# Kernel optimization log

Measured on AMD Instinct MI355X. Metric: run time of the kernel, lower is better.

Reference implementation:

```python
import jax, jax.numpy as jnp
import numpy as np

DIM = 768      # model dim (c_s)
C_PAIR = 128   # pair channels (c_z)
H = 16         # heads
C = DIM // H   # per-head dim (48)
INF = 1e8
EPS = 1e-5


def _ln(x, w=None, b=None):
    mu = jnp.mean(x, axis=-1, keepdims=True)
    var = jnp.mean(jnp.square(x - mu), axis=-1, keepdims=True)
    y = (x - mu) * jax.lax.rsqrt(var + EPS)
    if w is not None:
        y = y * w
    if b is not None:
        y = y + b
    return y


def setup_inputs() -> dict:
    key = jax.random.key(0)
    ks = jax.random.split(key, 12)
    B, S, N = 1, 2, 1024
    sd = 1.0 / np.sqrt(DIM)
    return {
        "single_repr": jax.random.normal(ks[0], (B, S, N, DIM), jnp.float32),
        "single_proj": jax.random.normal(ks[1], (B, S, N, DIM), jnp.float32),
        "pair_repr": jax.random.normal(ks[2], (B, N, N, C_PAIR), jnp.float32),
        "mask": jnp.ones((B, N), jnp.float32),
        # AdaLN params: LN(a) has no affine; LN(s) is scale-only; gate Linear + skip LinearNoBias
        "adaln_s_w": jnp.ones((DIM,), jnp.float32),
        "adaln_gate_w": (jax.random.normal(ks[3], (DIM, DIM), jnp.float32) * sd),
        "adaln_gate_b": jnp.zeros((DIM,), jnp.float32),
        "adaln_skip_w": (jax.random.normal(ks[4], (DIM, DIM), jnp.float32) * sd),
        # Attention params (q/k/v no bias, sigmoid gate linear, output linear)
        "wq": jax.random.normal(ks[5], (DIM, DIM), jnp.float32) * sd,
        "wk": jax.random.normal(ks[6], (DIM, DIM), jnp.float32) * sd,
        "wv": jax.random.normal(ks[7], (DIM, DIM), jnp.float32) * sd,
        "w_gate": jax.random.normal(ks[8], (DIM, DIM), jnp.float32) * sd,
        "b_gate": jnp.ones((DIM,), jnp.float32),
        "wo": jax.random.normal(ks[9], (DIM, DIM), jnp.float32) * sd,
        "bo": jnp.zeros((DIM,), jnp.float32),
        # proj_pair_bias: LayerNorm(c_pair) + LinearNoBias(c_pair, H)
        "pair_ln_w": jnp.ones((C_PAIR,), jnp.float32),
        "pair_ln_b": jnp.zeros((C_PAIR,), jnp.float32),
        "w_pair": jax.random.normal(ks[10], (C_PAIR, H), jnp.float32) / np.sqrt(C_PAIR),
        # output gating linear (bias initialized to -2 as in the module)
        "w_out": jax.random.normal(ks[11], (DIM, DIM), jnp.float32) * sd,
        "b_out": jnp.full((DIM,), -2.0, jnp.float32),
    }


def reference(single_repr, single_proj, pair_repr, mask,
              adaln_s_w, adaln_gate_w, adaln_gate_b, adaln_skip_w,
              wq, wk, wv, w_gate, b_gate, wo, bo,
              pair_ln_w, pair_ln_b, w_pair, w_out, b_out):
    B, S, N, _ = single_repr.shape
    # AdaLN input gating: a = sigmoid(Lin(LN_scale(s))) * LN(a) + LinNoBias(LN_scale(s))
    a = _ln(single_repr)
    s = _ln(single_proj, adaln_s_w)
    a = jax.nn.sigmoid(s @ adaln_gate_w + adaln_gate_b) * a + s @ adaln_skip_w
    # Biases: mask_bias [B,1,1,1,N]; pair_bias [B,1,H,N,N]
    mask_bias = (INF * (mask - 1.0))[:, None, None, None, :]
    pair_bias = _ln(pair_repr, pair_ln_w, pair_ln_b) @ w_pair      # [B,N,N,H]
    pair_bias = jnp.transpose(pair_bias, (0, 3, 1, 2))[:, None]    # [B,1,H,N,N]
    # Multi-head attention with fused biases
    q = (a @ wq).reshape(B, S, N, H, C)
    k = (a @ wk).reshape(B, S, N, H, C)
    v = (a @ wv).reshape(B, S, N, H, C)
    scale = 1.0 / np.sqrt(C)
    scores = jnp.einsum('bsqhc,bskhc->bshqk', q, k) * scale + mask_bias + pair_bias
    attn = jax.nn.softmax(scores, axis=-1)
    o = jnp.einsum('bshqk,bskhc->bsqhc', attn, v).reshape(B, S, N, DIM)
    # sigmoid gating on attention output, then output projection
    o = o * jax.nn.sigmoid(a @ w_gate + b_gate)
    o = o @ wo + bo
    # final sigmoid output gating (input_gating=True)
    out = jax.nn.sigmoid(o @ w_out + b_out) * o
    return out
```

## Files before the change

### kernel.cpp

```cpp
#include <hip/hip_runtime.h>

#define NROWS 2048
#define NN    1024
#define DIMM  768
#define HEADS 16
#define CH    48
#define CPAIR 128

typedef unsigned short u16;
typedef unsigned int   u32;
typedef __attribute__((ext_vector_type(8))) short short8;
typedef __attribute__((ext_vector_type(4))) float f32x4;

__device__ __forceinline__ float sigm(float x){ return 1.0f/(1.0f+__expf(-x)); }
__device__ __forceinline__ u16 f2bf(float x){
    u32 u = __float_as_uint(x);
    u32 r = u + 0x7FFFu + ((u>>16)&1u);
    return (u16)(r>>16);
}
__device__ __forceinline__ float bf2f(u16 h){ return __uint_as_float(((u32)h)<<16); }
__device__ __forceinline__ void bfsplit(float x, u16& hi, u16& lo){
    hi = f2bf(x);
    lo = f2bf(x - bf2f(hi));
}

__global__ __launch_bounds__(256) void k_ln_single(
    const float* __restrict__ srep, const float* __restrict__ sproj,
    const float* __restrict__ sw, float* __restrict__ a_ln,
    u16* __restrict__ shi, u16* __restrict__ slo)
{
    int r = blockIdx.x, t = threadIdx.x;
    const float* xa = srep  + (size_t)r*DIMM;
    const float* xs = sproj + (size_t)r*DIMM;
    float va[3], vs[3];
    float sa=0.f,qa=0.f,ss=0.f,qs=0.f;
    #pragma unroll
    for (int i=0;i<3;i++){ float x=xa[t+256*i]; va[i]=x; sa+=x; qa+=x*x; }
    #pragma unroll
    for (int i=0;i<3;i++){ float x=xs[t+256*i]; vs[i]=x; ss+=x; qs+=x*x; }
    #pragma unroll
    for (int off=32; off>=1; off>>=1){
        sa += __shfl_xor(sa,off); qa += __shfl_xor(qa,off);
        ss += __shfl_xor(ss,off); qs += __shfl_xor(qs,off);
    }
    __shared__ float red[16];
    int w = t>>6;
    if ((t&63)==0){ red[w*4+0]=sa; red[w*4+1]=qa; red[w*4+2]=ss; red[w*4+3]=qs; }
    __syncthreads();
    sa = red[0]+red[4]+red[8]+red[12];
    qa = red[1]+red[5]+red[9]+red[13];
    ss = red[2]+red[6]+red[10]+red[14];
    qs = red[3]+red[7]+red[11]+red[15];
    float mua=sa*(1.f/768.f), mus=ss*(1.f/768.f);
    float rva=rsqrtf(fmaxf(qa*(1.f/768.f)-mua*mua,0.f)+1e-5f);
    float rvs=rsqrtf(fmaxf(qs*(1.f/768.f)-mus*mus,0.f)+1e-5f);
    #pragma unroll
    for (int i=0;i<3;i++){
        int c=t+256*i;
        size_t idx=(size_t)r*DIMM+c;
        a_ln[idx]=(va[i]-mua)*rva;
        float sv=(vs[i]-mus)*rvs*sw[c];
        u16 h,l; bfsplit(sv,h,l);
        shi[idx]=h; slo[idx]=l;
    }
}

__global__ __launch_bounds__(256) void k_wsplit(
    const float* __restrict__ w0, const float* __restrict__ w1,
    const float* __restrict__ w2, const float* __restrict__ w3,
    const float* __restrict__ w4, const float* __restrict__ w5,
    const float* __restrict__ w6, const float* __restrict__ w7,
    u16* __restrict__ wt)
{
    __shared__ float tile[64][68];
    int n0 = blockIdx.x*64, k0 = blockIdx.y*64, z = blockIdx.z;
    const float* src;
    switch(z){
        case 0: src=w0; break; case 1: src=w1; break;
        case 2: src=w2; break; case 3: src=w3; break;
        case 4: src=w4; break; case 5: src=w5; break;
        case 6: src=w6; break; default: src=w7; break;
    }
    int t = threadIdx.x;
    #pragma unroll
    for (int it=0; it<4; it++){
        int idx = t + it*256;
        int kr = idx>>4, nc = (idx&15)*4;
        float4 v = *(const float4*)(src + (size_t)(k0+kr)*DIMM + n0+nc);
        *(float4*)(&tile[kr][nc]) = v;
    }
    __syncthreads();
    u16* wth = wt + (size_t)z*2*589824;
    u16* wtl = wth + 589824;
    #pragma unroll
    for (int it=0; it<4; it++){
        int idx = t + it*256;
        int nr = idx>>4, kc = (idx&15)*4;
        ushort4 h4, l4;
        u16 h,l;
        bfsplit(tile[kc+0][nr],h,l); h4.x=h; l4.x=l;
        bfsplit(tile[kc+1][nr],h,l); h4.y=h; l4.y=l;
        bfsplit(tile[kc+2][nr],h,l); h4.z=h; l4.z=l;
        bfsplit(tile[kc+3][nr],h,l); h4.w=h; l4.w=l;
        size_t o = (size_t)(n0+nr)*DIMM + k0+kc;
        *(ushort4*)(wth + o) = h4;
        *(ushort4*)(wtl + o) = l4;
    }
}

__global__ void k_pair_pre(const float* __restrict__ lnw, const float* __restrict__ lnb,
                           const float* __restrict__ wp, float* __restrict__ wpc,
                           float* __restrict__ csb)
{
    int t = threadIdx.x;
    for (int i=t;i<2048;i+=256) wpc[i] = lnw[i>>4]*wp[i];
    if (t<16){
        float cs=0.f,b0=0.f;
        for (int c=0;c<128;c++){ cs += lnw[c]*wp[c*16+t]; b0 += lnb[c]*wp[c*16+t]; }
        csb[t]=cs; csb[16+t]=b0;
    }
}

__device__ __forceinline__ void fma16(float yc, const float* __restrict__ wrow,
                                      float acc[16])
{
    const float4* wr = (const float4*)wrow;
    float4 w0=wr[0], w1=wr[1], w2=wr[2], w3=wr[3];
    acc[0]+=yc*w0.x;  acc[1]+=yc*w0.y;  acc[2]+=yc*w0.z;  acc[3]+=yc*w0.w;
    acc[4]+=yc*w1.x;  acc[5]+=yc*w1.y;  acc[6]+=yc*w1.z;  acc[7]+=yc*w1.w;
    acc[8]+=yc*w2.x;  acc[9]+=yc*w2.y;  acc[10]+=yc*w2.z; acc[11]+=yc*w2.w;
    acc[12]+=yc*w3.x; acc[13]+=yc*w3.y; acc[14]+=yc*w3.z; acc[15]+=yc*w3.w;
}

__global__ __launch_bounds__(256, 4) void k_pair_bias(
    const float* __restrict__ pair, const float* __restrict__ wpc,
    const float* __restrict__ csb, const float* __restrict__ mask,
    u16* __restrict__ pb)
{
    int row = blockIdx.x*256 + threadIdx.x;
    int j = row & (NN-1);
    const float4* x4 = (const float4*)(pair + (size_t)row*CPAIR);
    float s=0.f, sq=0.f;
    float acc[16];
    #pragma unroll
    for (int h=0;h<16;h++) acc[h]=0.f;
    #pragma unroll 4
    for (int i=0;i<32;i++){
        float4 v = x4[i];
        s  += v.x+v.y+v.z+v.w;
        sq += v.x*v.x+v.y*v.y+v.z*v.z+v.w*v.w;
        fma16(v.x, wpc + (4*i+0)*16, acc);
        fma16(v.y, wpc + (4*i+1)*16, acc);
        fma16(v.z, wpc + (4*i+2)*16, acc);
        fma16(v.w, wpc + (4*i+3)*16, acc);
    }
    float mu = s*(1.f/128.f);
    float rs = rsqrtf(fmaxf(sq*(1.f/128.f)-mu*mu,0.f)+1e-5f);
    float mb = 1e8f*(mask[j]-1.f);
    #pragma unroll
    for (int h=0;h<16;h++){
        float outv = (acc[h]-mu*csb[h])*rs + csb[16+h] + mb;
        pb[((size_t)h<<20) + row] = f2bf(outv);
    }
}

template<int NB, int EPI>
__global__ __launch_bounds__(256) void k_gemm(
    const u16* __restrict__ Ahp, const u16* __restrict__ Alp,
    const u16* __restrict__ B0h, const u16* __restrict__ B0l,
    const u16* __restrict__ B1h, const u16* __restrict__ B1l,
    const float* __restrict__ e0, const float* __restrict__ e1,
    float* __restrict__ o0, float* __restrict__ o1,
    u16* __restrict__ oh, u16* __restrict__ ol)
{
    __shared__ u16 lA[2][128][40];
    __shared__ u16 lB[NB][2][64][40];
    int m0 = blockIdx.x*128, n0 = blockIdx.y*64;
    int t = threadIdx.x, lane = t&63, w = t>>6;
    int fr = lane&15, fg = lane>>4;
    f32x4 acc[NB][2][4];
    #pragma unroll
    for (int i=0;i<NB;i++)
        #pragma unroll
        for (int mf=0;mf<2;mf++)
            #pragma unroll
            for (int nf=0;nf<4;nf++) acc[i][mf][nf] = (f32x4){0.f,0.f,0.f,0.f};

    for (int k0=0; k0<DIMM; k0+=32){
        #pragma unroll
        for (int it=0; it<4; it++){
            int s = t + it*256;
            int plane = s>>9, s2 = s&511;
            int row = s2>>2, seg = (s2&3)*8;
            const u16* src = plane ? Alp : Ahp;
            *(int4*)(&lA[plane][row][seg]) =
                *(const int4*)(src + (size_t)(m0+row)*DIMM + k0 + seg);
        }
        #pragma unroll
        for (int i=0;i<NB;i++){
            const u16* bh = i ? B1h : B0h;
            const u16* bl = i ? B1l : B0l;
            #pragma unroll
            for (int it=0; it<2; it++){
                int s = t + it*256;
                int plane = s>>8, s2 = s&255;
                int row = s2>>2, seg = (s2&3)*8;
                const u16* src = plane ? bl : bh;
                *(int4*)(&lB[i][plane][row][seg]) =
                    *(const int4*)(src + (size_t)(n0+row)*DIMM + k0 + seg);
            }
        }
        __syncthreads();
        short8 a_h0 = *(const short8*)(&lA[0][w*32+fr][fg*8]);
        short8 a_h1 = *(const short8*)(&lA[0][w*32+16+fr][fg*8]);
        short8 a_l0 = *(const short8*)(&lA[1][w*32+fr][fg*8]);
        short8 a_l1 = *(const short8*)(&lA[1][w*32+16+fr][fg*8]);
        #pragma unroll
        for (int nf=0;nf<4;nf++){
            #pragma unroll
            for (int i=0;i<NB;i++){
                short8 b_h = *(const short8*)(&lB[i][0][nf*16+fr][fg*8]);
                short8 b_l = *(const short8*)(&lB[i][1][nf*16+fr][fg*8]);
                acc[i][0][nf] = __builtin_amdgcn_mfma_f32_16x16x32_bf16(a_h0, b_h, acc[i][0][nf], 0,0,0);
                acc[i][0][nf] = __builtin_amdgcn_mfma_f32_16x16x32_bf16(a_h0, b_l, acc[i][0][nf], 0,0,0);
                acc[i][0][nf] = __builtin_amdgcn_mfma_f32_16x16x32_bf16(a_l0, b_h, acc[i][0][nf], 0,0,0);
                acc[i][1][nf] = __builtin_amdgcn_mfma_f32_16x16x32_bf16(a_h1, b_h, acc[i][1][nf], 0,0,0);
                acc[i][1][nf] = __builtin_amdgcn_mfma_f32_16x16x32_bf16(a_h1, b_l, acc[i][1][nf], 0,0,0);
                acc[i][1][nf] = __builtin_amdgcn_mfma_f32_16x16x32_bf16(a_l1, b_h, acc[i][1][nf], 0,0,0);
            }
        }
        __syncthreads();
    }
    #pragma unroll
    for (int mf=0;mf<2;mf++){
        #pragma unroll
        for (int nf=0;nf<4;nf++){
            #pragma unroll
            for (int r=0;r<4;r++){
                int row = m0 + w*32 + mf*16 + fg*4 + r;
                int col = n0 + nf*16 + fr;
                size_t idx = (size_t)row*DIMM + col;
                float c0 = acc[0][mf][nf][r];
                if (EPI==0){
                    float c1 = acc[1][mf][nf][r];
                    float v = sigm(c0 + e0[col]) * e1[idx] + c1;
                    u16 h,l; bfsplit(v,h,l); oh[idx]=h; ol[idx]=l;
                } else if (EPI==1){
                    u16* kh_ = (u16*)o0; u16* kl_ = (u16*)o1;
                    int s2 = row>>10, n = row&(NN-1);
                    int hh2 = col/CH, cc = col-hh2*CH;
                    size_t pidx = ((size_t)(s2*HEADS+hh2)*NN + n)*CH + cc;
                    u16 hx,lx;
                    bfsplit(c0*0.14433756729740643f, hx,lx);
                    oh[pidx]=hx; ol[pidx]=lx;
                    float c1 = acc[1][mf][nf][r];
                    bfsplit(c1,hx,lx);
                    kh_[pidx]=hx; kl_[pidx]=lx;
                } else if (EPI==2){
                    int s2 = row>>10, n = row&(NN-1);
                    int hh2 = col/CH, cc = col-hh2*CH;
                    size_t vidx = ((size_t)(s2*HEADS+hh2)*CH + cc)*NN + n;
                    u16 hx,lx; bfsplit(c0,hx,lx);
                    oh[vidx]=hx; ol[vidx]=lx;
                    float c1 = acc[1][mf][nf][r];
                    o0[idx] = sigm(c1 + e0[col]);
                } else if (EPI==3){
                    float v = c0 + e0[col];
                    u16 h,l; bfsplit(v,h,l); oh[idx]=h; ol[idx]=l;
                } else {
                    float o2v = bf2f(Ahp[idx]) + bf2f(Alp[idx]);
                    o0[idx] = sigm(c0 + e0[col]) * o2v;
                }
            }
        }
    }
}

__global__ __launch_bounds__(256) void k_attn(
    const u16* __restrict__ qah, const u16* __restrict__ qal,
    const u16* __restrict__ kah, const u16* __restrict__ kal,
    const u16* __restrict__ vth, const u16* __restrict__ vtl,
    const u16* __restrict__ pb, const float* __restrict__ g,
    u16* __restrict__ oghi, u16* __restrict__ oglo)
{
    __shared__ u16 lQh[64][72], lQl[64][72], lKh[64][72], lKl[64][72];
    __shared__ u16 lVh[48][72], lVl[48][72];
    __shared__ u16 lP[4][16][72];
    int t = threadIdx.x, lane = t&63, w = t>>6;
    int fr = lane&15, fg = lane>>4;
    int m0 = blockIdx.x*64;
    int sh = blockIdx.y, s = sh>>4, h = sh&15;
    size_t qkbase = (size_t)sh*NN*CH;
    size_t vbase  = (size_t)sh*CH*NN;

    {
        int row = t>>2, which = t&3;
        u16* dst = (which==0)? &lQh[row][48] : (which==1)? &lQl[row][48] :
                   (which==2)? &lKh[row][48] : &lKl[row][48];
        *(int4*)dst     = make_int4(0,0,0,0);
        *(int4*)(dst+8) = make_int4(0,0,0,0);
    }
    {
        const u16* src0 = qah + qkbase + (size_t)m0*CH;
        const u16* src1 = qal + qkbase + (size_t)m0*CH;
        #pragma unroll
        for (int it=0; it<3; it++){
            int sid = t + it*256;
            int plane = sid>=384; int s2 = plane ? sid-384 : sid;
            int row = s2/6, seg = s2-row*6;
            int4 v = *(const int4*)((plane?src1:src0) + row*CH + seg*8);
            u16 (*dq)[72] = plane? lQl : lQh;
            *(int4*)(&dq[row][seg*8]) = v;
        }
    }
    __syncthreads();
    short8 aqh0 = *(const short8*)(&lQh[w*16+fr][fg*8]);
    short8 aqh1 = *(const short8*)(&lQh[w*16+fr][32+fg*8]);
    short8 aql0 = *(const short8*)(&lQl[w*16+fr][fg*8]);
    short8 aql1 = *(const short8*)(&lQl[w*16+fr][32+fg*8]);

    f32x4 acc_o[3];
    #pragma unroll
    for (int i=0;i<3;i++) acc_o[i]=(f32x4){0.f,0.f,0.f,0.f};
    float m[4], l[4];
    #pragma unroll
    for (int r=0;r<4;r++){ m[r]=-3e38f; l[r]=0.f; }
    int qrow_base = m0 + w*16 + fg*4;
    const u16* pbq = pb + ((size_t)h<<20) + (size_t)qrow_base*NN + fr;

    for (int kt=0; kt<16; kt++){
        int k0 = kt*64;
        int4 kreg[3], vreg[3];
        const u16* ksrc0 = kah + qkbase + (size_t)k0*CH;
        const u16* ksrc1 = kal + qkbase + (size_t)k0*CH;
        const u16* vsrc0 = vth + vbase + k0;
        const u16* vsrc1 = vtl + vbase + k0;
        #pragma unroll
        for (int it=0; it<3; it++){
            int sid = t + it*256;
            int plane = sid>=384; int s2 = plane ? sid-384 : sid;
            int row = s2/6, seg = s2-row*6;
            kreg[it] = *(const int4*)((plane?ksrc1:ksrc0) + row*CH + seg*8);
            int rowv = s2>>3, segv = s2&7;
            vreg[it] = *(const int4*)((plane?vsrc1:vsrc0) + (size_t)rowv*NN + segv*8);
        }
        u16 pbv[4][4];
        #pragma unroll
        for (int r=0;r<4;r++)
            #pragma unroll
            for (int nf=0;nf<4;nf++)
                pbv[r][nf] = pbq[(size_t)r*NN + k0 + nf*16];
        __syncthreads();
        #pragma unroll
        for (int it=0; it<3; it++){
            int sid = t + it*256;
            int plane = sid>=384; int s2 = plane ? sid-384 : sid;
            int row = s2/6, seg = s2-row*6;
            u16 (*dk)[72] = plane? lKl : lKh;
            *(int4*)(&dk[row][seg*8]) = kreg[it];
            int rowv = s2>>3, segv = s2&7;
            u16 (*dv)[72] = plane? lVl : lVh;
            *(int4*)(&dv[rowv][segv*8]) = vreg[it];
        }
        __syncthreads();
        f32x4 sc[4];
        #pragma unroll
        for (int nf=0;nf<4;nf++){
            short8 bh0 = *(const short8*)(&lKh[nf*16+fr][fg*8]);
            short8 bh1 = *(const short8*)(&lKh[nf*16+fr][32+fg*8]);
            short8 bl0 = *(const short8*)(&lKl[nf*16+fr][fg*8]);
            short8 bl1 = *(const short8*)(&lKl[nf*16+fr][32+fg*8]);
            f32x4 a = (f32x4){0.f,0.f,0.f,0.f};
            a = __builtin_amdgcn_mfma_f32_16x16x32_bf16(aqh0, bh0, a, 0,0,0);
            a = __builtin_amdgcn_mfma_f32_16x16x32_bf16(aqh1, bh1, a, 0,0,0);
            a = __builtin_amdgcn_mfma_f32_16x16x32_bf16(aqh0, bl0, a, 0,0,0);
            a = __builtin_amdgcn_mfma_f32_16x16x32_bf16(aqh1, bl1, a, 0,0,0);
            a = __builtin_amdgcn_mfma_f32_16x16x32_bf16(aql0, bh0, a, 0,0,0);
            a = __builtin_amdgcn_mfma_f32_16x16x32_bf16(aql1, bh1, a, 0,0,0);
            sc[nf]=a;
        }
        float mn[4];
        #pragma unroll
        for (int r=0;r<4;r++){
            float v0 = sc[0][r]+bf2f(pbv[r][0]);
            float v1 = sc[1][r]+bf2f(pbv[r][1]);
            float v2 = sc[2][r]+bf2f(pbv[r][2]);
            float v3 = sc[3][r]+bf2f(pbv[r][3]);
            sc[0][r]=v0; sc[1][r]=v1; sc[2][r]=v2; sc[3][r]=v3;
            float mx = fmaxf(fmaxf(v0,v1),fmaxf(v2,v3));
            mx = fmaxf(mx, __shfl_xor(mx,1,64));
            mx = fmaxf(mx, __shfl_xor(mx,2,64));
            mx = fmaxf(mx, __shfl_xor(mx,4,64));
            mx = fmaxf(mx, __shfl_xor(mx,8,64));
            mn[r]=mx;
        }
        #pragma unroll
        for (int r=0;r<4;r++){
            float mnew = fmaxf(m[r], mn[r]);
            float corr = __expf(m[r]-mnew);
            m[r]=mnew;
            float ps=0.f;
            #pragma unroll
            for (int nf=0;nf<4;nf++){
                float p = __expf(sc[nf][r]-mnew);
                u16 pu = f2bf(p);
                ps += bf2f(pu);
                lP[w][fg*4+r][nf*16+fr] = pu;
            }
            l[r] = l[r]*corr + ps;
            acc_o[0][r]*=corr; acc_o[1][r]*=corr; acc_o[2][r]*=corr;
        }
        short8 pa0 = *(const short8*)(&lP[w][fr][fg*8]);
        short8 pa1 = *(const short8*)(&lP[w][fr][32+fg*8]);
        #pragma unroll
        for (int cf=0;cf<3;cf++){
            short8 vh0 = *(const short8*)(&lVh[cf*16+fr][fg*8]);
            short8 vh1 = *(const short8*)(&lVh[cf*16+fr][32+fg*8]);
            short8 vl0 = *(const short8*)(&lVl[cf*16+fr][fg*8]);
            short8 vl1 = *(const short8*)(&lVl[cf*16+fr][32+fg*8]);
            acc_o[cf] = __builtin_amdgcn_mfma_f32_16x16x32_bf16(pa0, vh0, acc_o[cf], 0,0,0);
            acc_o[cf] = __builtin_amdgcn_mfma_f32_16x16x32_bf16(pa1, vh1, acc_o[cf], 0,0,0);
            acc_o[cf] = __builtin_amdgcn_mfma_f32_16x16x32_bf16(pa0, vl0, acc_o[cf], 0,0,0);
            acc_o[cf] = __builtin_amdgcn_mfma_f32_16x16x32_bf16(pa1, vl1, acc_o[cf], 0,0,0);
        }
    }
    float rl[4];
    #pragma unroll
    for (int r=0;r<4;r++){
        float lv = l[r];
        lv += __shfl_xor(lv,1,64);
        lv += __shfl_xor(lv,2,64);
        lv += __shfl_xor(lv,4,64);
        lv += __shfl_xor(lv,8,64);
        rl[r] = 1.f/lv;
    }
    #pragma unroll
    for (int cf=0;cf<3;cf++){
        #pragma unroll
        for (int r=0;r<4;r++){
            size_t orow = ((size_t)(s*NN + m0 + w*16 + fg*4 + r))*DIMM + h*CH + cf*16 + fr;
            float val = acc_o[cf][r]*rl[r] * g[orow];
            u16 hh,ll; bfsplit(val,hh,ll);
            oghi[orow]=hh; oglo[orow]=ll;
        }
    }
}

extern "C" void kernel_launch(void* const* d_in, const int* in_sizes, int n_in,
                              void* d_out, int out_size, void* d_ws, size_t ws_size,
                              hipStream_t stream)
{
    const float* srep   = (const float*)d_in[0];
    const float* sproj  = (const float*)d_in[1];
    const float* pair   = (const float*)d_in[2];
    const float* mask   = (const float*)d_in[3];
    const float* s_w    = (const float*)d_in[4];
    const float* gate_w = (const float*)d_in[5];
    const float* gate_b = (const float*)d_in[6];
    const float* skip_w = (const float*)d_in[7];
    const float* wq     = (const float*)d_in[8];
    const float* wk     = (const float*)d_in[9];
    const float* wv     = (const float*)d_in[10];
    const float* w_gate = (const float*)d_in[11];
    const float* b_gate = (const float*)d_in[12];
    const float* wo     = (const float*)d_in[13];
    const float* bo     = (const float*)d_in[14];
    const float* plnw   = (const float*)d_in[15];
    const float* plnb   = (const float*)d_in[16];
    const float* w_pair = (const float*)d_in[17];
    const float* w_out  = (const float*)d_in[18];
    const float* b_out  = (const float*)d_in[19];
    float* out = (float*)d_out;

    const size_t T  = (size_t)NROWS*DIMM;
    const size_t W  = (size_t)DIMM*DIMM;
    const size_t PB = (size_t)HEADS*NN*NN;

    char* p = (char*)d_ws;
    float* a_ln = (float*)p; p += T*4;
    float* g    = (float*)p; p += T*4;
    float* wpc  = (float*)p; p += 2048*4;
    float* csb  = (float*)p; p += 32*4;
    u16* shi  = (u16*)p; p += T*2;
    u16* slo  = (u16*)p; p += T*2;
    u16* ahi  = (u16*)p; p += T*2;
    u16* alo  = (u16*)p; p += T*2;
    u16* oghi = (u16*)p; p += T*2;
    u16* oglo = (u16*)p; p += T*2;
    u16* o2hi = (u16*)p; p += T*2;
    u16* o2lo = (u16*)p; p += T*2;
    u16* qah  = (u16*)p; p += T*2;
    u16* qal  = (u16*)p; p += T*2;
    u16* kah  = (u16*)p; p += T*2;
    u16* kal  = (u16*)p; p += T*2;
    u16* vth  = (u16*)p; p += T*2;
    u16* vtl  = (u16*)p; p += T*2;
    u16* pbias= (u16*)p; p += PB*2;
    u16* wt   = (u16*)p; p += 16*W*2;

    #define WH(i) (wt + (size_t)(i)*2*W)
    #define WL(i) (wt + (size_t)(i)*2*W + W)

    k_wsplit<<<dim3(12,12,8), 256, 0, stream>>>(
        gate_w, skip_w, wq, wk, wv, w_gate, wo, w_out, wt);
    k_ln_single<<<NROWS, 256, 0, stream>>>(srep, sproj, s_w, a_ln, shi, slo);
    k_pair_pre<<<1, 256, 0, stream>>>(plnw, plnb, w_pair, wpc, csb);
    k_pair_bias<<<(NN*NN)/256, 256, 0, stream>>>(pair, wpc, csb, mask, pbias);

    dim3 gg(NROWS/128, DIMM/64);
    k_gemm<2,0><<<gg, 256, 0, stream>>>(shi, slo, WH(0), WL(0), WH(1), WL(1),
                                        gate_b, a_ln, nullptr, nullptr, ahi, alo);
    k_gemm<2,1><<<gg, 256, 0, stream>>>(ahi, alo, WH(2), WL(2), WH(3), WL(3),
                                        nullptr, nullptr, (float*)kah, (float*)kal, qah, qal);
    k_gemm<2,2><<<gg, 256, 0, stream>>>(ahi, alo, WH(4), WL(4), WH(5), WL(5),
                                        b_gate, nullptr, g, nullptr, vth, vtl);

    k_attn<<<dim3(NN/64, 2*HEADS), 256, 0, stream>>>(
        qah, qal, kah, kal, vth, vtl, pbias, g, oghi, oglo);

    k_gemm<1,3><<<gg, 256, 0, stream>>>(oghi, oglo, WH(6), WL(6), nullptr, nullptr,
                                        bo, nullptr, nullptr, nullptr, o2hi, o2lo);
    k_gemm<1,4><<<gg, 256, 0, stream>>>(o2hi, o2lo, WH(7), WL(7), nullptr, nullptr,
                                        b_out, nullptr, out, nullptr, nullptr, nullptr);
    #undef WH
    #undef WL
}
```

Measured before the change: 419.2 us.

## Prefetch GEMM K-tiles into registers and merge QK/VG projection launches

```diff
diff --git a/kernel.cpp b/kernel.cpp
--- a/kernel.cpp
+++ b/kernel.cpp
@@ -164,37 +164,26 @@
     }
 }
 
-template<int NB, int EPI>
-__global__ __launch_bounds__(256) void k_gemm(
+template<int NB>
+__device__ __forceinline__ void gemm_main(
     const u16* __restrict__ Ahp, const u16* __restrict__ Alp,
     const u16* __restrict__ B0h, const u16* __restrict__ B0l,
     const u16* __restrict__ B1h, const u16* __restrict__ B1l,
-    const float* __restrict__ e0, const float* __restrict__ e1,
-    float* __restrict__ o0, float* __restrict__ o1,
-    u16* __restrict__ oh, u16* __restrict__ ol)
-{
-    __shared__ u16 lA[2][128][40];
-    __shared__ u16 lB[NB][2][64][40];
-    int m0 = blockIdx.x*128, n0 = blockIdx.y*64;
-    int t = threadIdx.x, lane = t&63, w = t>>6;
+    int m0, int n0, int t,
+    u16 (&lA)[2][128][40], u16 (&lB)[NB][2][64][40],
+    f32x4 (&acc)[NB][2][4])
+{
+    int lane = t&63, w = t>>6;
     int fr = lane&15, fg = lane>>4;
-    f32x4 acc[NB][2][4];
-    #pragma unroll
-    for (int i=0;i<NB;i++)
-        #pragma unroll
-        for (int mf=0;mf<2;mf++)
-            #pragma unroll
-            for (int nf=0;nf<4;nf++) acc[i][mf][nf] = (f32x4){0.f,0.f,0.f,0.f};
-
-    for (int k0=0; k0<DIMM; k0+=32){
+    int4 pa[4], pbr[NB][2];
+
+    auto loadk = [&](int k0){
         #pragma unroll
         for (int it=0; it<4; it++){
             int s = t + it*256;
-            int plane = s>>9, s2 = s&511;
+            int pl = s>>9, s2 = s&511;
             int row = s2>>2, seg = (s2&3)*8;
-            const u16* src = plane ? Alp : Ahp;
-            *(int4*)(&lA[plane][row][seg]) =
-                *(const int4*)(src + (size_t)(m0+row)*DIMM + k0 + seg);
+            pa[it] = *(const int4*)((pl?Alp:Ahp) + (size_t)(m0+row)*DIMM + k0 + seg);
         }
         #pragma unroll
         for (int i=0;i<NB;i++){
@@ -203,14 +192,37 @@
             #pragma unroll
             for (int it=0; it<2; it++){
                 int s = t + it*256;
-                int plane = s>>8, s2 = s&255;
+                int pl = s>>8, s2 = s&255;
                 int row = s2>>2, seg = (s2&3)*8;
-                const u16* src = plane ? bl : bh;
-                *(int4*)(&lB[i][plane][row][seg]) =
-                    *(const int4*)(src + (size_t)(n0+row)*DIMM + k0 + seg);
+                pbr[i][it] = *(const int4*)((pl?bl:bh) + (size_t)(n0+row)*DIMM + k0 + seg);
             }
         }
+    };
+    auto storek = [&](){
+        #pragma unroll
+        for (int it=0; it<4; it++){
+            int s = t + it*256;
+            int pl = s>>9, s2 = s&511;
+            int row = s2>>2, seg = (s2&3)*8;
+            *(int4*)(&lA[pl][row][seg]) = pa[it];
+        }
+        #pragma unroll
+        for (int i=0;i<NB;i++){
+            #pragma unroll
+            for (int it=0; it<2; it++){
+                int s = t + it*256;
+                int pl = s>>8, s2 = s&255;
+                int row = s2>>2, seg = (s2&3)*8;
+                *(int4*)(&lB[i][pl][row][seg]) = pbr[i][it];
+            }
+        }
+    };
+
+    loadk(0);
+    storek();
+    for (int ks=0; ks<24; ks++){
         __syncthreads();
+        if (ks<23) loadk((ks+1)*32);
         short8 a_h0 = *(const short8*)(&lA[0][w*32+fr][fg*8]);
         short8 a_h1 = *(const short8*)(&lA[0][w*32+16+fr][fg*8]);
         short8 a_l0 = *(const short8*)(&lA[1][w*32+fr][fg*8]);
@@ -229,8 +241,37 @@
                 acc[i][1][nf] = __builtin_amdgcn_mfma_f32_16x16x32_bf16(a_l1, b_h, acc[i][1][nf], 0,0,0);
             }
         }
-        __syncthreads();
-    }
+        if (ks<23){
+            __syncthreads();
+            storek();
+        }
+    }
+}
+
+template<int NB, int EPI>
+__global__ __launch_bounds__(256) void k_gemm(
+    const u16* __restrict__ Ahp, const u16* __restrict__ Alp,
+    const u16* __restrict__ B0h, const u16* __restrict__ B0l,
+    const u16* __restrict__ B1h, const u16* __restrict__ B1l,
+    const float* __restrict__ e0, const float* __restrict__ e1,
+    float* __restrict__ o0, float* __restrict__ o1,
+    u16* __restrict__ oh, u16* __restrict__ ol)
+{
+    __shared__ u16 lA[2][128][40];
+    __shared__ u16 lB[NB][2][64][40];
+    int m0 = blockIdx.x*128, n0 = blockIdx.y*64;
+    int t = threadIdx.x, lane = t&63, w = t>>6;
+    int fr = lane&15, fg = lane>>4;
+    f32x4 acc[NB][2][4];
+    #pragma unroll
+    for (int i=0;i<NB;i++)
+        #pragma unroll
+        for (int mf=0;mf<2;mf++)
+            #pragma unroll
+            for (int nf=0;nf<4;nf++) acc[i][mf][nf] = (f32x4){0.f,0.f,0.f,0.f};
+
+    gemm_main<NB>(Ahp, Alp, B0h, B0l, B1h, B1l, m0, n0, t, lA, lB, acc);
+
     #pragma unroll
     for (int mf=0;mf<2;mf++){
         #pragma unroll
@@ -245,31 +286,75 @@
                     float c1 = acc[1][mf][nf][r];
                     float v = sigm(c0 + e0[col]) * e1[idx] + c1;
                     u16 h,l; bfsplit(v,h,l); oh[idx]=h; ol[idx]=l;
-                } else if (EPI==1){
-                    u16* kh_ = (u16*)o0; u16* kl_ = (u16*)o1;
-                    int s2 = row>>10, n = row&(NN-1);
-                    int hh2 = col/CH, cc = col-hh2*CH;
-                    size_t pidx = ((size_t)(s2*HEADS+hh2)*NN + n)*CH + cc;
-                    u16 hx,lx;
-                    bfsplit(c0*0.14433756729740643f, hx,lx);
-                    oh[pidx]=hx; ol[pidx]=lx;
-                    float c1 = acc[1][mf][nf][r];
-                    bfsplit(c1,hx,lx);
-                    kh_[pidx]=hx; kl_[pidx]=lx;
-                } else if (EPI==2){
-                    int s2 = row>>10, n = row&(NN-1);
-                    int hh2 = col/CH, cc = col-hh2*CH;
-                    size_t vidx = ((size_t)(s2*HEADS+hh2)*CH + cc)*NN + n;
-                    u16 hx,lx; bfsplit(c0,hx,lx);
-                    oh[vidx]=hx; ol[vidx]=lx;
-                    float c1 = acc[1][mf][nf][r];
-                    o0[idx] = sigm(c1 + e0[col]);
                 } else if (EPI==3){
                     float v = c0 + e0[col];
                     u16 h,l; bfsplit(v,h,l); oh[idx]=h; ol[idx]=l;
                 } else {
                     float o2v = bf2f(Ahp[idx]) + bf2f(Alp[idx]);
                     o0[idx] = sigm(c0 + e0[col]) * o2v;
+                }
+            }
+        }
+    }
+}
+
+__global__ __launch_bounds__(256) void k_gemm_qkvg(
+    const u16* __restrict__ Ahp, const u16* __restrict__ Alp,
+    const u16* __restrict__ wqh, const u16* __restrict__ wql,
+    const u16* __restrict__ wkh, const u16* __restrict__ wkl,
+    const u16* __restrict__ wvh, const u16* __restrict__ wvl,
+    const u16* __restrict__ wgh, const u16* __restrict__ wgl,
+    const float* __restrict__ bgate,
+    u16* __restrict__ qah, u16* __restrict__ qal,
+    u16* __restrict__ kah, u16* __restrict__ kal,
+    u16* __restrict__ vth, u16* __restrict__ vtl,
+    float* __restrict__ g)
+{
+    __shared__ u16 lA[2][128][40];
+    __shared__ u16 lB[2][2][64][40];
+    int m0 = blockIdx.x*128, n0 = blockIdx.y*64;
+    int z = blockIdx.z;
+    const u16* B0h = z ? wvh : wqh;
+    const u16* B0l = z ? wvl : wql;
+    const u16* B1h = z ? wgh : wkh;
+    const u16* B1l = z ? wgl : wkl;
+    int t = threadIdx.x, lane = t&63, w = t>>6;
+    int fr = lane&15, fg = lane>>4;
+    f32x4 acc[2][2][4];
+    #pragma unroll
+    for (int i=0;i<2;i++)
+        #pragma unroll
+        for (int mf=0;mf<2;mf++)
+            #pragma unroll
+            for (int nf=0;nf<4;nf++) acc[i][mf][nf] = (f32x4){0.f,0.f,0.f,0.f};
+
+    gemm_main<2>(Ahp, Alp, B0h, B0l, B1h, B1l, m0, n0, t, lA, lB, acc);
+
+    #pragma unroll
+    for (int mf=0;mf<2;mf++){
+        #pragma unroll
+        for (int nf=0;nf<4;nf++){
+            #pragma unroll
+            for (int r=0;r<4;r++){
+                int row = m0 + w*32 + mf*16 + fg*4 + r;
+                int col = n0 + nf*16 + fr;
+                size_t idx = (size_t)row*DIMM + col;
+                int s2 = row>>10, n = row&(NN-1);
+                int hh2 = col/CH, cc = col-hh2*CH;
+                float c0 = acc[0][mf][nf][r];
+                float c1 = acc[1][mf][nf][r];
+                if (z==0){
+                    size_t pidx = ((size_t)(s2*HEADS+hh2)*NN + n)*CH + cc;
+                    u16 hx,lx;
+                    bfsplit(c0*0.14433756729740643f, hx,lx);
+                    qah[pidx]=hx; qal[pidx]=lx;
+                    bfsplit(c1,hx,lx);
+                    kah[pidx]=hx; kal[pidx]=lx;
+                } else {
+                    size_t vidx = ((size_t)(s2*HEADS+hh2)*CH + cc)*NN + n;
+                    u16 hx,lx; bfsplit(c0,hx,lx);
+                    vth[vidx]=hx; vtl[vidx]=lx;
+                    g[idx] = sigm(c1 + bgate[col]);
                 }
             }
         }
@@ -510,10 +595,9 @@
     dim3 gg(NROWS/128, DIMM/64);
     k_gemm<2,0><<<gg, 256, 0, stream>>>(shi, slo, WH(0), WL(0), WH(1), WL(1),
                                         gate_b, a_ln, nullptr, nullptr, ahi, alo);
-    k_gemm<2,1><<<gg, 256, 0, stream>>>(ahi, alo, WH(2), WL(2), WH(3), WL(3),
-                                        nullptr, nullptr, (float*)kah, (float*)kal, qah, qal);
-    k_gemm<2,2><<<gg, 256, 0, stream>>>(ahi, alo, WH(4), WL(4), WH(5), WL(5),
-                                        b_gate, nullptr, g, nullptr, vth, vtl);
+    k_gemm_qkvg<<<dim3(NROWS/128, DIMM/64, 2), 256, 0, stream>>>(
+        ahi, alo, WH(2), WL(2), WH(3), WL(3), WH(4), WL(4), WH(5), WL(5),
+        b_gate, qah, qal, kah, kal, vth, vtl, g);
 
     k_attn<<<dim3(NN/64, 2*HEADS), 256, 0, stream>>>(
         qah, qal, kah, kal, vth, vtl, pbias, g, oghi, oglo);
```

Result: slower. 559.1 us (+33.4%).
